# Kernel tuning notes

Hardware: AMD Instinct MI355X
Metric: run time of the kernel (lower is better)

## Reference

```python
import jax, jax.numpy as jnp
import numpy as np

QMAX = 127.0

def quantize_int8(x):
    # symmetric per-row (per-token) int8 quantization
    scale = jnp.max(jnp.abs(x), axis=-1, keepdims=True) / QMAX  # [N,1]
    scale = jnp.maximum(scale, 1e-8)
    q = jnp.clip(jnp.round(x / scale), -QMAX, QMAX).astype(jnp.int8)
    return q, scale


def setup_inputs() -> dict:
    key = jax.random.key(0)
    k1, k2 = jax.random.split(key)
    in_features, out_features = 4096, 4096
    x = jax.random.normal(k1, (4, 2048, in_features), dtype=jnp.float32)
    # weight buffer: randint(1, 128) int8, shape (out, in)
    weight = jax.random.randint(k2, (out_features, in_features), 1, 128, dtype=jnp.int32).astype(jnp.int8)
    weight_scale = jnp.ones((1,), dtype=jnp.float32)
    return {"x": x, "weight": weight, "weight_scale": weight_scale}


def reference(x, weight, weight_scale):
    x_shape = x.shape
    xf = x.reshape(-1, x_shape[-1])  # [N, in]
    q, scale_x = quantize_int8(xf)
    acc = jnp.matmul(q, weight.T, preferred_element_type=jnp.int32)  # [N, out]
    y = acc.astype(jnp.float32) * scale_x * weight_scale[0]
    return y.reshape(*x_shape[:-1], -1)
```

## Files before the change

kernel.cpp:

```cpp
#include <hip/hip_runtime.h>
#include <cstdint>

typedef int v4i __attribute__((ext_vector_type(4)));

#define K_DIM 4096
#define BM 128
#define BN 128
#define BK 64

__global__ __launch_bounds__(256) void pack_weight(
    const int* __restrict__ w32, int8_t* __restrict__ w8, int total16)
{
    const int i = blockIdx.x * 256 + threadIdx.x;
    if (i >= total16) return;
    const v4i* src = reinterpret_cast<const v4i*>(w32) + i * 4;
    v4i out;
#pragma unroll
    for (int j = 0; j < 4; ++j) {
        const v4i v = src[j];
        out[j] = (v.x & 0xff) | ((v.y & 0xff) << 8) |
                 ((v.z & 0xff) << 16) | ((unsigned)(v.w & 0xff) << 24);
    }
    reinterpret_cast<v4i*>(w8)[i] = out;
}

__global__ __launch_bounds__(256) void quant_rows(
    const float* __restrict__ x, int8_t* __restrict__ q,
    float* __restrict__ scales)
{
    const int row = blockIdx.x;
    const int t   = threadIdx.x;
    const float4* xr4 = reinterpret_cast<const float4*>(x + (size_t)row * K_DIM);

    float4 v[4];
    float m = 0.0f;
#pragma unroll
    for (int i = 0; i < 4; ++i) {
        v[i] = xr4[i * 256 + t];
        m = fmaxf(m, fmaxf(fmaxf(fabsf(v[i].x), fabsf(v[i].y)),
                           fmaxf(fabsf(v[i].z), fabsf(v[i].w))));
    }
#pragma unroll
    for (int off = 32; off >= 1; off >>= 1)
        m = fmaxf(m, __shfl_xor(m, off, 64));

    __shared__ float wmax[4];
    if ((t & 63) == 0) wmax[t >> 6] = m;
    __syncthreads();
    const float am = fmaxf(fmaxf(wmax[0], wmax[1]), fmaxf(wmax[2], wmax[3]));
    const float s  = fmaxf(am / 127.0f, 1e-8f);
    if (t == 0) scales[row] = s;

    int* qi = reinterpret_cast<int*>(q + (size_t)row * K_DIM);
#pragma unroll
    for (int i = 0; i < 4; ++i) {
        const float e[4] = {v[i].x, v[i].y, v[i].z, v[i].w};
        unsigned packed = 0;
#pragma unroll
        for (int j = 0; j < 4; ++j) {
            float r = rintf(e[j] / s);
            r = fminf(fmaxf(r, -127.0f), 127.0f);
            packed |= ((unsigned)((int)r & 0xff)) << (8 * j);
        }
        qi[i * 256 + t] = (int)packed;
    }
}

__global__ __launch_bounds__(256, 2) void gemm_i8(
    const int8_t* __restrict__ A,
    const int8_t* __restrict__ B,
    const float* __restrict__ sA,
    const float* __restrict__ wsc,
    float* __restrict__ C,
    int M, int N)
{
    __shared__ int8_t ldsA[BM * BK];
    __shared__ int8_t ldsB[BN * BK];

    const int t    = threadIdx.x;
    const int lane = t & 63;
    const int wid  = t >> 6;
    const int wr   = wid >> 1;
    const int wc   = wid & 1;

    const int brow = blockIdx.y * BM;
    const int bcol = blockIdx.x * BN;

    const float ws = wsc[0];

    v4i acc[4][4];
#pragma unroll
    for (int i = 0; i < 4; ++i)
#pragma unroll
        for (int j = 0; j < 4; ++j)
            acc[i][j] = (v4i){0, 0, 0, 0};

    for (int kt = 0; kt < K_DIM; kt += BK) {
        __syncthreads();
#pragma unroll
        for (int b = 0; b < 2; ++b) {
            const int idx = b * 256 + t;
            const int row = idx >> 2;
            const int seg = (idx & 3) * 16;
            const int8_t* ga = A + (size_t)(brow + row) * K_DIM + kt + seg;
            const int8_t* gb = B + (size_t)(bcol + row) * K_DIM + kt + seg;
            __builtin_amdgcn_global_load_lds(
                (const __attribute__((address_space(1))) void*)ga,
                (__attribute__((address_space(3))) void*)(ldsA + idx * 16),
                16, 0, 0);
            __builtin_amdgcn_global_load_lds(
                (const __attribute__((address_space(1))) void*)gb,
                (__attribute__((address_space(3))) void*)(ldsB + idx * 16),
                16, 0, 0);
        }
        __syncthreads();

        v4i a[4], bf[4];
#pragma unroll
        for (int rb = 0; rb < 4; ++rb) {
            const int r = wr * 64 + rb * 16 + (lane & 15);
            a[rb] = *reinterpret_cast<const v4i*>(&ldsA[r * BK + (lane >> 4) * 16]);
        }
#pragma unroll
        for (int cb = 0; cb < 4; ++cb) {
            const int c = wc * 64 + cb * 16 + (lane & 15);
            bf[cb] = *reinterpret_cast<const v4i*>(&ldsB[c * BK + (lane >> 4) * 16]);
        }
#pragma unroll
        for (int rb = 0; rb < 4; ++rb)
#pragma unroll
            for (int cb = 0; cb < 4; ++cb)
                acc[rb][cb] = __builtin_amdgcn_mfma_i32_16x16x64_i8(
                    a[rb], bf[cb], acc[rb][cb], 0, 0, 0);
    }

#pragma unroll
    for (int rb = 0; rb < 4; ++rb) {
        const int rbase = brow + wr * 64 + rb * 16 + (lane >> 4) * 4;
        float sc[4];
#pragma unroll
        for (int j = 0; j < 4; ++j) sc[j] = sA[rbase + j] * ws;
#pragma unroll
        for (int cb = 0; cb < 4; ++cb) {
            const int col = bcol + wc * 64 + cb * 16 + (lane & 15);
#pragma unroll
            for (int j = 0; j < 4; ++j)
                C[(size_t)(rbase + j) * N + col] = (float)acc[rb][cb][j] * sc[j];
        }
    }
}

extern "C" void kernel_launch(void* const* d_in, const int* in_sizes, int n_in,
                              void* d_out, int out_size, void* d_ws, size_t ws_size,
                              hipStream_t stream) {
    const float* x      = (const float*)d_in[0];
    const int*   w32    = (const int*)d_in[1];
    const float* wscale = (const float*)d_in[2];
    float*       out    = (float*)d_out;

    const int M = in_sizes[0] / K_DIM;
    const int N = in_sizes[1] / K_DIM;

    int8_t* q      = (int8_t*)d_ws;
    float*  scales = (float*)((char*)d_ws + (size_t)M * K_DIM);
    int8_t* w8     = (int8_t*)((char*)d_ws + (size_t)M * K_DIM + (size_t)M * sizeof(float));

    const int total16 = (N * K_DIM) / 16;
    pack_weight<<<(total16 + 255) / 256, 256, 0, stream>>>(w32, w8, total16);

    quant_rows<<<M, 256, 0, stream>>>(x, q, scales);

    dim3 grid(N / BN, M / BM);
    gemm_i8<<<grid, 256, 0, stream>>>(q, w8, scales, wscale, out, M, N);
}
```

Measured before the change: 233.0 us.

## Triple-buffer 256x256 int8 GEMM tiles with swizzled LDS and XCD block remap

Replaces the single-buffered 128x128 GEMM with a 256x256 tile computed by 512 threads. Three LDS stages are fed by global_load_lds prefetches two K-steps ahead, interleaved with split MFMA phases under s_setprio. It also XOR-swizzles the LDS layout to cut bank conflicts and remaps block IDs across XCDs for L2 locality. The aim is to hide global-load latency and raise data reuse per tile, at the cost of more registers (128 accumulator VGPRs per lane), 96KB of LDS per block, and only 128 blocks to spread across the CUs.

```diff
diff --git a/kernel.cpp b/kernel.cpp
--- a/kernel.cpp
+++ b/kernel.cpp
@@ -4,9 +4,12 @@
 typedef int v4i __attribute__((ext_vector_type(4)));
 
 #define K_DIM 4096
-#define BM 128
-#define BN 128
+#define BM 256
+#define BN 256
 #define BK 64
+#define NT (K_DIM / BK)
+#define TILE_BYTES (BM * BK)
+#define BUF_STRIDE (2 * TILE_BYTES)
 
 __global__ __launch_bounds__(256) void pack_weight(
     const int* __restrict__ w32, int8_t* __restrict__ w8, int total16)
@@ -66,7 +69,7 @@
     }
 }
 
-__global__ __launch_bounds__(256, 2) void gemm_i8(
+__global__ __launch_bounds__(512, 2) void gemm_i8(
     const int8_t* __restrict__ A,
     const int8_t* __restrict__ B,
     const float* __restrict__ sA,
@@ -74,80 +77,144 @@
     float* __restrict__ C,
     int M, int N)
 {
-    __shared__ int8_t ldsA[BM * BK];
-    __shared__ int8_t ldsB[BN * BK];
+    __shared__ int8_t lds[3 * BUF_STRIDE];
 
     const int t    = threadIdx.x;
     const int lane = t & 63;
-    const int wid  = t >> 6;
-    const int wr   = wid >> 1;
-    const int wc   = wid & 1;
-
-    const int brow = blockIdx.y * BM;
-    const int bcol = blockIdx.x * BN;
-
-    const float ws = wsc[0];
-
-    v4i acc[4][4];
-#pragma unroll
-    for (int i = 0; i < 4; ++i)
-#pragma unroll
-        for (int j = 0; j < 4; ++j)
-            acc[i][j] = (v4i){0, 0, 0, 0};
-
-    for (int kt = 0; kt < K_DIM; kt += BK) {
-        __syncthreads();
-#pragma unroll
-        for (int b = 0; b < 2; ++b) {
-            const int idx = b * 256 + t;
-            const int row = idx >> 2;
-            const int seg = (idx & 3) * 16;
-            const int8_t* ga = A + (size_t)(brow + row) * K_DIM + kt + seg;
-            const int8_t* gb = B + (size_t)(bcol + row) * K_DIM + kt + seg;
-            __builtin_amdgcn_global_load_lds(
-                (const __attribute__((address_space(1))) void*)ga,
-                (__attribute__((address_space(3))) void*)(ldsA + idx * 16),
-                16, 0, 0);
-            __builtin_amdgcn_global_load_lds(
-                (const __attribute__((address_space(1))) void*)gb,
-                (__attribute__((address_space(3))) void*)(ldsB + idx * 16),
-                16, 0, 0);
+    const int w    = t >> 6;
+    const int wr   = w >> 2;
+    const int wc   = w & 3;
+
+    const int nwg = gridDim.x;
+    int bid = blockIdx.x;
+    if ((nwg & 7) == 0) bid = (bid & 7) * (nwg >> 3) + (bid >> 3);
+    const int ntn  = N / BN;
+    const int brow = (bid / ntn) * BM;
+    const int bcol = (bid % ntn) * BN;
+
+    const int idx0 = t;
+    const int idx1 = t + 512;
+    const int r0 = idx0 >> 2, r1 = idx1 >> 2;
+    const int c0 = (((idx0 & 3) ^ ((r0 >> 1) & 3)) << 4);
+    const int c1 = (((idx1 & 3) ^ ((r1 >> 1) & 3)) << 4);
+    const int8_t* gA0 = A + (size_t)(brow + r0) * K_DIM + c0;
+    const int8_t* gA1 = A + (size_t)(brow + r1) * K_DIM + c1;
+    const int8_t* gB0 = B + (size_t)(bcol + r0) * K_DIM + c0;
+    const int8_t* gB1 = B + (size_t)(bcol + r1) * K_DIM + c1;
+    const int dst0 = idx0 * 16, dst1 = idx1 * 16;
+
+#define GLDS(gp, off) \
+    __builtin_amdgcn_global_load_lds( \
+        (const __attribute__((address_space(1))) void*)(gp), \
+        (__attribute__((address_space(3))) void*)(lds + (off)), 16, 0, 0)
+#define STAGE_A(buf, tt) do { \
+    GLDS(gA0 + (size_t)(tt) * BK, (buf) * BUF_STRIDE + dst0); \
+    GLDS(gA1 + (size_t)(tt) * BK, (buf) * BUF_STRIDE + dst1); } while (0)
+#define STAGE_B(buf, tt) do { \
+    GLDS(gB0 + (size_t)(tt) * BK, (buf) * BUF_STRIDE + TILE_BYTES + dst0); \
+    GLDS(gB1 + (size_t)(tt) * BK, (buf) * BUF_STRIDE + TILE_BYTES + dst1); } while (0)
+
+    const int c16 = lane >> 4;
+    int offA[2][4], offB[4];
+#pragma unroll
+    for (int mh = 0; mh < 2; ++mh)
+#pragma unroll
+        for (int m = 0; m < 4; ++m) {
+            const int row = wr * 128 + mh * 64 + m * 16 + (lane & 15);
+            offA[mh][m] = row * BK + ((c16 ^ ((row >> 1) & 3)) << 4);
         }
-        __syncthreads();
-
-        v4i a[4], bf[4];
-#pragma unroll
-        for (int rb = 0; rb < 4; ++rb) {
-            const int r = wr * 64 + rb * 16 + (lane & 15);
-            a[rb] = *reinterpret_cast<const v4i*>(&ldsA[r * BK + (lane >> 4) * 16]);
+#pragma unroll
+    for (int n = 0; n < 4; ++n) {
+        const int row = wc * 64 + n * 16 + (lane & 15);
+        offB[n] = TILE_BYTES + row * BK + ((c16 ^ ((row >> 1) & 3)) << 4);
+    }
+
+    v4i acc[8][4];
+#pragma unroll
+    for (int m = 0; m < 8; ++m)
+#pragma unroll
+        for (int n = 0; n < 4; ++n)
+            acc[m][n] = (v4i){0, 0, 0, 0};
+
+    STAGE_A(0, 0); STAGE_B(0, 0);
+    STAGE_A(1, 1); STAGE_B(1, 1);
+    asm volatile("s_waitcnt vmcnt(4)" ::: "memory");
+    __builtin_amdgcn_s_barrier();
+
+#define MFMA_Q(BASE) do { \
+    acc[BASE+0][0] = __builtin_amdgcn_mfma_i32_16x16x64_i8(a0, b0, acc[BASE+0][0], 0,0,0); \
+    acc[BASE+0][1] = __builtin_amdgcn_mfma_i32_16x16x64_i8(a0, b1, acc[BASE+0][1], 0,0,0); \
+    acc[BASE+0][2] = __builtin_amdgcn_mfma_i32_16x16x64_i8(a0, b2, acc[BASE+0][2], 0,0,0); \
+    acc[BASE+0][3] = __builtin_amdgcn_mfma_i32_16x16x64_i8(a0, b3, acc[BASE+0][3], 0,0,0); \
+    acc[BASE+1][0] = __builtin_amdgcn_mfma_i32_16x16x64_i8(a1, b0, acc[BASE+1][0], 0,0,0); \
+    acc[BASE+1][1] = __builtin_amdgcn_mfma_i32_16x16x64_i8(a1, b1, acc[BASE+1][1], 0,0,0); \
+    acc[BASE+1][2] = __builtin_amdgcn_mfma_i32_16x16x64_i8(a1, b2, acc[BASE+1][2], 0,0,0); \
+    acc[BASE+1][3] = __builtin_amdgcn_mfma_i32_16x16x64_i8(a1, b3, acc[BASE+1][3], 0,0,0); \
+    acc[BASE+2][0] = __builtin_amdgcn_mfma_i32_16x16x64_i8(a2, b0, acc[BASE+2][0], 0,0,0); \
+    acc[BASE+2][1] = __builtin_amdgcn_mfma_i32_16x16x64_i8(a2, b1, acc[BASE+2][1], 0,0,0); \
+    acc[BASE+2][2] = __builtin_amdgcn_mfma_i32_16x16x64_i8(a2, b2, acc[BASE+2][2], 0,0,0); \
+    acc[BASE+2][3] = __builtin_amdgcn_mfma_i32_16x16x64_i8(a2, b3, acc[BASE+2][3], 0,0,0); \
+    acc[BASE+3][0] = __builtin_amdgcn_mfma_i32_16x16x64_i8(a3, b0, acc[BASE+3][0], 0,0,0); \
+    acc[BASE+3][1] = __builtin_amdgcn_mfma_i32_16x16x64_i8(a3, b1, acc[BASE+3][1], 0,0,0); \
+    acc[BASE+3][2] = __builtin_amdgcn_mfma_i32_16x16x64_i8(a3, b2, acc[BASE+3][2], 0,0,0); \
+    acc[BASE+3][3] = __builtin_amdgcn_mfma_i32_16x16x64_i8(a3, b3, acc[BASE+3][3], 0,0,0); \
+    } while (0)
+
+    int cur = 0, nx = 2;
+    for (int tt = 0; tt < NT; ++tt) {
+        const int8_t* bufc = lds + cur * BUF_STRIDE;
+        v4i a0, a1, a2, a3, b0, b1, b2, b3;
+        a0 = *(const v4i*)(bufc + offA[0][0]);
+        a1 = *(const v4i*)(bufc + offA[0][1]);
+        a2 = *(const v4i*)(bufc + offA[0][2]);
+        a3 = *(const v4i*)(bufc + offA[0][3]);
+        b0 = *(const v4i*)(bufc + offB[0]);
+        b1 = *(const v4i*)(bufc + offB[1]);
+        b2 = *(const v4i*)(bufc + offB[2]);
+        b3 = *(const v4i*)(bufc + offB[3]);
+        if (tt + 2 < NT) STAGE_A(nx, tt + 2);
+        __builtin_amdgcn_s_barrier();
+        asm volatile("s_waitcnt lgkmcnt(0)" ::: "memory");
+        __builtin_amdgcn_s_setprio(1);
+        MFMA_Q(0);
+        __builtin_amdgcn_s_setprio(0);
+        __builtin_amdgcn_s_barrier();
+        a0 = *(const v4i*)(bufc + offA[1][0]);
+        a1 = *(const v4i*)(bufc + offA[1][1]);
+        a2 = *(const v4i*)(bufc + offA[1][2]);
+        a3 = *(const v4i*)(bufc + offA[1][3]);
+        if (tt + 2 < NT) STAGE_B(nx, tt + 2);
+        __builtin_amdgcn_s_barrier();
+        asm volatile("s_waitcnt lgkmcnt(0)" ::: "memory");
+        __builtin_amdgcn_s_setprio(1);
+        MFMA_Q(4);
+        __builtin_amdgcn_s_setprio(0);
+        if (tt + 2 < NT)      asm volatile("s_waitcnt vmcnt(4)" ::: "memory");
+        else if (tt + 1 < NT) asm volatile("s_waitcnt vmcnt(0)" ::: "memory");
+        __builtin_amdgcn_s_barrier();
+        cur = (cur == 2) ? 0 : cur + 1;
+        nx  = (nx  == 2) ? 0 : nx  + 1;
+    }
+
+    const float wsv = wsc[0];
+#pragma unroll
+    for (int m = 0; m < 8; ++m) {
+        const int rbase = brow + wr * 128 + m * 16 + (lane >> 4) * 4;
+        float sc[4];
+#pragma unroll
+        for (int j = 0; j < 4; ++j) sc[j] = sA[rbase + j] * wsv;
+#pragma unroll
+        for (int n = 0; n < 4; ++n) {
+            const int col = bcol + wc * 64 + n * 16 + (lane & 15);
+#pragma unroll
+            for (int j = 0; j < 4; ++j)
+                C[(size_t)(rbase + j) * N + col] = (float)acc[m][n][j] * sc[j];
         }
-#pragma unroll
-        for (int cb = 0; cb < 4; ++cb) {
-            const int c = wc * 64 + cb * 16 + (lane & 15);
-            bf[cb] = *reinterpret_cast<const v4i*>(&ldsB[c * BK + (lane >> 4) * 16]);
-        }
-#pragma unroll
-        for (int rb = 0; rb < 4; ++rb)
-#pragma unroll
-            for (int cb = 0; cb < 4; ++cb)
-                acc[rb][cb] = __builtin_amdgcn_mfma_i32_16x16x64_i8(
-                    a[rb], bf[cb], acc[rb][cb], 0, 0, 0);
-    }
-
-#pragma unroll
-    for (int rb = 0; rb < 4; ++rb) {
-        const int rbase = brow + wr * 64 + rb * 16 + (lane >> 4) * 4;
-        float sc[4];
-#pragma unroll
-        for (int j = 0; j < 4; ++j) sc[j] = sA[rbase + j] * ws;
-#pragma unroll
-        for (int cb = 0; cb < 4; ++cb) {
-            const int col = bcol + wc * 64 + cb * 16 + (lane & 15);
-#pragma unroll
-            for (int j = 0; j < 4; ++j)
-                C[(size_t)(rbase + j) * N + col] = (float)acc[rb][cb][j] * sc[j];
-        }
-    }
+    }
+#undef GLDS
+#undef STAGE_A
+#undef STAGE_B
+#undef MFMA_Q
 }
 
 extern "C" void kernel_launch(void* const* d_in, const int* in_sizes, int n_in,
@@ -170,6 +237,6 @@
 
     quant_rows<<<M, 256, 0, stream>>>(x, q, scales);
 
-    dim3 grid(N / BN, M / BM);
-    gemm_i8<<<grid, 256, 0, stream>>>(q, w8, scales, wscale, out, M, N);
-}
+    const int nblk = (M / BM) * (N / BN);
+    gemm_i8<<<nblk, 512, 0, stream>>>(q, w8, scales, wscale, out, M, N);
+}
```

Result: faster. 200.5 us (-14.0%).

## Enlarge GEMM tiles to 256x256 with 4-stage LDS pipeline, swizzle, and XCD remap

Applied to the files above, without the earlier changes.

Reworks the int8 GEMM to use 256x256 block tiles with a 4-buffer LDS ring, so global-to-LDS loads run three tiles ahead. LDS reads and MFMAs are interleaved phase by phase with register double-buffering of B fragments. It also XOR-swizzles the LDS layout to avoid bank conflicts and remaps block ids across XCDs for better L2 locality. The costs are 128 KB of LDS, 64 accumulators per thread, and occupancy limited to one block per CU, with only 128 blocks in the grid.

```diff
diff --git a/kernel.cpp b/kernel.cpp
--- a/kernel.cpp
+++ b/kernel.cpp
@@ -4,9 +4,12 @@
 typedef int v4i __attribute__((ext_vector_type(4)));
 
 #define K_DIM 4096
-#define BM 128
-#define BN 128
+#define BM 256
+#define BN 256
 #define BK 64
+#define NT (K_DIM / BK)
+#define BUFS 32768
+#define NBUF 4
 
 __global__ __launch_bounds__(256) void pack_weight(
     const int* __restrict__ w32, int8_t* __restrict__ w8, int total16)
@@ -66,7 +69,7 @@
     }
 }
 
-__global__ __launch_bounds__(256, 2) void gemm_i8(
+__global__ __launch_bounds__(256, 1) void gemm_i8(
     const int8_t* __restrict__ A,
     const int8_t* __restrict__ B,
     const float* __restrict__ sA,
@@ -74,80 +77,126 @@
     float* __restrict__ C,
     int M, int N)
 {
-    __shared__ int8_t ldsA[BM * BK];
-    __shared__ int8_t ldsB[BN * BK];
+    __shared__ int8_t lds[NBUF * BUFS];
 
     const int t    = threadIdx.x;
     const int lane = t & 63;
-    const int wid  = t >> 6;
-    const int wr   = wid >> 1;
-    const int wc   = wid & 1;
-
-    const int brow = blockIdx.y * BM;
-    const int bcol = blockIdx.x * BN;
-
-    const float ws = wsc[0];
-
-    v4i acc[4][4];
-#pragma unroll
-    for (int i = 0; i < 4; ++i)
-#pragma unroll
-        for (int j = 0; j < 4; ++j)
-            acc[i][j] = (v4i){0, 0, 0, 0};
-
-    for (int kt = 0; kt < K_DIM; kt += BK) {
-        __syncthreads();
-#pragma unroll
-        for (int b = 0; b < 2; ++b) {
-            const int idx = b * 256 + t;
-            const int row = idx >> 2;
-            const int seg = (idx & 3) * 16;
-            const int8_t* ga = A + (size_t)(brow + row) * K_DIM + kt + seg;
-            const int8_t* gb = B + (size_t)(bcol + row) * K_DIM + kt + seg;
-            __builtin_amdgcn_global_load_lds(
-                (const __attribute__((address_space(1))) void*)ga,
-                (__attribute__((address_space(3))) void*)(ldsA + idx * 16),
-                16, 0, 0);
-            __builtin_amdgcn_global_load_lds(
-                (const __attribute__((address_space(1))) void*)gb,
-                (__attribute__((address_space(3))) void*)(ldsB + idx * 16),
-                16, 0, 0);
+    const int w    = t >> 6;
+    const int wr   = w >> 1;
+    const int wc   = w & 1;
+
+    const int nwg = gridDim.x;
+    int bid = blockIdx.x;
+    if ((nwg & 7) == 0) bid = (bid & 7) * (nwg >> 3) + (bid >> 3);
+    const int ntn  = N / BN;
+    const int brow = (bid / ntn) * BM;
+    const int bcol = (bid % ntn) * BN;
+
+    const int8_t* gsrc[8];
+    int ldst[8];
+#pragma unroll
+    for (int c = 0; c < 4; ++c) {
+        const int idx  = c * 256 + t;
+        const int row  = idx >> 2;
+        const int colq = (((idx & 3) ^ ((row >> 1) & 3)) << 4);
+        gsrc[c]     = A + (size_t)(brow + row) * K_DIM + colq;
+        ldst[c]     = idx * 16;
+        gsrc[4 + c] = B + (size_t)(bcol + row) * K_DIM + colq;
+        ldst[4 + c] = 16384 + idx * 16;
+    }
+
+#define GLDS(gp, off) \
+    __builtin_amdgcn_global_load_lds( \
+        (const __attribute__((address_space(1))) void*)(gp), \
+        (__attribute__((address_space(3))) void*)(lds + (off)), 16, 0, 0)
+
+    const int l15 = lane & 15;
+    const unsigned swz = ((unsigned)((lane >> 4) ^ ((l15 >> 1) & 3))) << 4;
+    const unsigned vA = (unsigned)((wr * 128 + l15) * 64) + swz;
+    const unsigned vB = 16384u + (unsigned)((wc * 128 + l15) * 64) + swz;
+
+    v4i acc[8][8];
+#pragma unroll
+    for (int m = 0; m < 8; ++m)
+#pragma unroll
+        for (int n = 0; n < 8; ++n)
+            acc[m][n] = (v4i){0, 0, 0, 0};
+
+    v4i aR[4], Ba[8], Bb[8];
+
+#pragma unroll
+    for (int c = 0; c < 8; ++c) GLDS(gsrc[c],            ldst[c]);
+#pragma unroll
+    for (int c = 0; c < 8; ++c) GLDS(gsrc[c] + BK,       BUFS + ldst[c]);
+#pragma unroll
+    for (int c = 0; c < 8; ++c) GLDS(gsrc[c] + 2 * BK, 2 * BUFS + ldst[c]);
+    asm volatile("s_waitcnt vmcnt(8)" ::: "memory");
+    __builtin_amdgcn_s_barrier();
+
+#pragma unroll
+    for (int n = 0; n < 8; ++n) Ba[n] = *(const v4i*)(lds + vB + n * 1024);
+    aR[0] = *(const v4i*)(lds + vA);
+    aR[1] = *(const v4i*)(lds + vA + 1024);
+
+#define MFMA8(P, BC) do { \
+    acc[P][0] = __builtin_amdgcn_mfma_i32_16x16x64_i8(aR[(P)&3], BC[0], acc[P][0], 0,0,0); \
+    acc[P][1] = __builtin_amdgcn_mfma_i32_16x16x64_i8(aR[(P)&3], BC[1], acc[P][1], 0,0,0); \
+    acc[P][2] = __builtin_amdgcn_mfma_i32_16x16x64_i8(aR[(P)&3], BC[2], acc[P][2], 0,0,0); \
+    acc[P][3] = __builtin_amdgcn_mfma_i32_16x16x64_i8(aR[(P)&3], BC[3], acc[P][3], 0,0,0); \
+    acc[P][4] = __builtin_amdgcn_mfma_i32_16x16x64_i8(aR[(P)&3], BC[4], acc[P][4], 0,0,0); \
+    acc[P][5] = __builtin_amdgcn_mfma_i32_16x16x64_i8(aR[(P)&3], BC[5], acc[P][5], 0,0,0); \
+    acc[P][6] = __builtin_amdgcn_mfma_i32_16x16x64_i8(aR[(P)&3], BC[6], acc[P][6], 0,0,0); \
+    acc[P][7] = __builtin_amdgcn_mfma_i32_16x16x64_i8(aR[(P)&3], BC[7], acc[P][7], 0,0,0); \
+    } while (0)
+
+#define PHASE(P, BC, BNX) do { \
+    if ((P) <= 5) aR[((P)+2)&3] = *(const v4i*)(bufc + vA + ((P)+2) * 1024); \
+    else if (notlast) aR[((P)+2)&3] = *(const v4i*)(bufn + vA + ((P)-6) * 1024); \
+    if (notlast) BNX[(P)] = *(const v4i*)(bufn + vB + (P) * 1024); \
+    if (more) GLDS(gsrc[(P)] + (size_t)T3 * BK, stoff + ldst[(P)]); \
+    MFMA8(P, BC); \
+    } while (0)
+
+#define TILE_BODY(T, BC, BNX) do { \
+    const int8_t* bufc = lds + cur * BUFS; \
+    const int8_t* bufn = lds + ((cur + 1) & 3) * BUFS; \
+    const unsigned stoff = (unsigned)(((cur + 3) & 3) * BUFS); \
+    const bool more = (T) + 3 < NT; \
+    const bool notlast = (T) + 1 < NT; \
+    const int T3 = (T) + 3; \
+    PHASE(0, BC, BNX); PHASE(1, BC, BNX); PHASE(2, BC, BNX); PHASE(3, BC, BNX); \
+    PHASE(4, BC, BNX); PHASE(5, BC, BNX); PHASE(6, BC, BNX); PHASE(7, BC, BNX); \
+    if (more)         asm volatile("s_waitcnt vmcnt(8)" ::: "memory"); \
+    else              asm volatile("s_waitcnt vmcnt(0)" ::: "memory"); \
+    if (notlast) __builtin_amdgcn_s_barrier(); \
+    cur = (cur + 1) & 3; \
+    } while (0)
+
+    int cur = 0;
+    for (int tt = 0; tt < NT; tt += 2) {
+        TILE_BODY(tt,     Ba, Bb);
+        TILE_BODY(tt + 1, Bb, Ba);
+    }
+
+    const float wsv = wsc[0];
+#pragma unroll
+    for (int m = 0; m < 8; ++m) {
+        const int rbase = brow + wr * 128 + m * 16 + (lane >> 4) * 4;
+        float sc[4];
+#pragma unroll
+        for (int j = 0; j < 4; ++j) sc[j] = sA[rbase + j] * wsv;
+#pragma unroll
+        for (int n = 0; n < 8; ++n) {
+            const int col = bcol + wc * 128 + n * 16 + l15;
+#pragma unroll
+            for (int j = 0; j < 4; ++j)
+                C[(size_t)(rbase + j) * N + col] = (float)acc[m][n][j] * sc[j];
         }
-        __syncthreads();
-
-        v4i a[4], bf[4];
-#pragma unroll
-        for (int rb = 0; rb < 4; ++rb) {
-            const int r = wr * 64 + rb * 16 + (lane & 15);
-            a[rb] = *reinterpret_cast<const v4i*>(&ldsA[r * BK + (lane >> 4) * 16]);
-        }
-#pragma unroll
-        for (int cb = 0; cb < 4; ++cb) {
-            const int c = wc * 64 + cb * 16 + (lane & 15);
-            bf[cb] = *reinterpret_cast<const v4i*>(&ldsB[c * BK + (lane >> 4) * 16]);
-        }
-#pragma unroll
-        for (int rb = 0; rb < 4; ++rb)
-#pragma unroll
-            for (int cb = 0; cb < 4; ++cb)
-                acc[rb][cb] = __builtin_amdgcn_mfma_i32_16x16x64_i8(
-                    a[rb], bf[cb], acc[rb][cb], 0, 0, 0);
-    }
-
-#pragma unroll
-    for (int rb = 0; rb < 4; ++rb) {
-        const int rbase = brow + wr * 64 + rb * 16 + (lane >> 4) * 4;
-        float sc[4];
-#pragma unroll
-        for (int j = 0; j < 4; ++j) sc[j] = sA[rbase + j] * ws;
-#pragma unroll
-        for (int cb = 0; cb < 4; ++cb) {
-            const int col = bcol + wc * 64 + cb * 16 + (lane & 15);
-#pragma unroll
-            for (int j = 0; j < 4; ++j)
-                C[(size_t)(rbase + j) * N + col] = (float)acc[rb][cb][j] * sc[j];
-        }
-    }
+    }
+#undef GLDS
+#undef MFMA8
+#undef PHASE
+#undef TILE_BODY
 }
 
 extern "C" void kernel_launch(void* const* d_in, const int* in_sizes, int n_in,
@@ -170,6 +219,6 @@
 
     quant_rows<<<M, 256, 0, stream>>>(x, q, scales);
 
-    dim3 grid(N / BN, M / BM);
-    gemm_i8<<<grid, 256, 0, stream>>>(q, w8, scales, wscale, out, M, N);
-}
+    const int nblk = (M / BM) * (N / BN);
+    gemm_i8<<<nblk, 256, 0, stream>>>(q, w8, scales, wscale, out, M, N);
+}
```

Result: slower. 404.9 us (+73.8%).
